# Optimization experiments

Measured on AMD Instinct MI355X. Metric: run time of the kernel, lower is better.

## Reference

```python
import jax, jax.numpy as jnp
import numpy as np

B, S, H, V = 16, 128, 512, 50000
N, R = 5, 2          # mem_size, read_heads
Wd = H               # memory cell width
EPS = 1e-6
XI_SIZES = [R * Wd, R, Wd, 1, Wd, Wd, R, 1, 1, 3 * R]
XI = int(np.sum(XI_SIZES))  # 2573


def oneplus(x):
    return 1.0 + jax.nn.softplus(x)


def content_weight(M, k, beta):
    # M: [B,N,Wd], k: [B,R,Wd], beta: [B,R] -> [B,R,N]
    Mn = M / (jnp.linalg.norm(M, axis=-1, keepdims=True) + EPS)
    kn = k / (jnp.linalg.norm(k, axis=-1, keepdims=True) + EPS)
    sim = jnp.einsum('brw,bnw->brn', kn, Mn)
    return jax.nn.softmax(beta[:, :, None] * sim, axis=-1)


def setup_inputs() -> dict:
    key = jax.random.key(0)
    ks = jax.random.split(key, 8)
    emb = jax.random.normal(ks[0], (V, H), jnp.float32) * 0.02
    emb = emb.at[0].set(0.0)  # PAD row
    return {
        'source': jax.random.randint(ks[1], (B, S), 0, V),
        'source_lengths': jax.random.randint(ks[2], (B,), 1, S + 1),
        'emb': emb,
        'W_ih': jax.random.normal(ks[3], (4 * H, H + R * Wd), jnp.float32) * 0.02,
        'W_hh': jax.random.normal(ks[4], (4 * H, H), jnp.float32) * 0.02,
        'b_lstm': jnp.zeros((4 * H,), jnp.float32),
        'W_int': jax.random.normal(ks[5], (H, XI), jnp.float32) * 0.02,
        'b_int': jnp.zeros((XI,), jnp.float32),
        'W_out': jax.random.normal(ks[6], (H + R * Wd, H), jnp.float32) * 0.02,
        'b_out': jnp.zeros((H,), jnp.float32),
    }


def dnc_forward(source, emb, W_ih, W_hh, b_lstm, W_int, b_int, W_out, b_out):
    x_emb = emb[source]  # [B,S,H] embedding lookup
    splits = np.cumsum(XI_SIZES)[:-1]
    eye = jnp.eye(N, dtype=jnp.float32)

    def step(carry, x_t):
        h, c, M, u, p, L, wr, ww, r = carry
        # LSTM controller: input = [embedded token; read vectors]
        xin = jnp.concatenate([x_t, r.reshape(-1, R * Wd)], axis=-1)
        gates = xin @ W_ih.T + h @ W_hh.T + b_lstm
        i_, f_, g_, o_ = jnp.split(gates, 4, axis=-1)
        c = jax.nn.sigmoid(f_) * c + jax.nn.sigmoid(i_) * jnp.tanh(g_)
        h = jax.nn.sigmoid(o_) * jnp.tanh(c)
        # interface vector
        xi = h @ W_int + b_int
        (rk, rb, wk, wb, e, v, fg, ga, gw, pi) = jnp.split(xi, splits, axis=-1)
        rk = rk.reshape(-1, R, Wd)
        rb = oneplus(rb)                       # [B,R]
        wb = oneplus(wb)                       # [B,1]
        e = jax.nn.sigmoid(e)                  # [B,Wd]
        fg = jax.nn.sigmoid(fg)                # [B,R]
        ga = jax.nn.sigmoid(ga)                # [B,1]
        gw = jax.nn.sigmoid(gw)                # [B,1]
        pi = jax.nn.softmax(pi.reshape(-1, R, 3), axis=-1)
        # usage / retention
        psi = jnp.prod(1.0 - fg[:, :, None] * wr, axis=1)        # [B,N]
        u = (u + ww - u * ww) * psi
        # allocation weighting (sort-based, irregular access)
        phi = jnp.argsort(u, axis=-1)
        u_s = jnp.take_along_axis(u, phi, axis=-1)
        excl = jnp.concatenate([jnp.ones_like(u_s[:, :1]), jnp.cumprod(u_s, axis=-1)[:, :-1]], axis=-1)
        a_s = (1.0 - u_s) * excl
        a = jnp.take_along_axis(a_s, jnp.argsort(phi, axis=-1), axis=-1)
        # write weighting
        cw = content_weight(M, wk[:, None, :], wb)[:, 0]         # [B,N]
        ww = gw * (ga * a + (1.0 - ga) * cw)
        # memory write
        M = M * (1.0 - ww[:, :, None] * e[:, None, :]) + ww[:, :, None] * v[:, None, :]
        # temporal link matrix + precedence
        L = (1.0 - ww[:, :, None] - ww[:, None, :]) * L + ww[:, :, None] * p[:, None, :]
        L = L * (1.0 - eye)
        p = (1.0 - ww.sum(-1, keepdims=True)) * p + ww
        # read weightings
        fw = jnp.einsum('bij,brj->bri', L, wr)
        bw = jnp.einsum('bji,brj->bri', L, wr)
        cr = content_weight(M, rk, rb)                           # [B,R,N]
        wr = pi[..., 0:1] * bw + pi[..., 1:2] * cr + pi[..., 2:3] * fw
        r = jnp.einsum('brn,bnw->brw', wr, M)                    # [B,R,Wd]
        out_t = jnp.concatenate([h, r.reshape(-1, R * Wd)], axis=-1) @ W_out + b_out
        return (h, c, M, u, p, L, wr, ww, r), out_t

    z = jnp.zeros
    init = (z((B, H)), z((B, H)), z((B, N, Wd)), z((B, N)), z((B, N)),
            z((B, N, N)), z((B, R, N)), z((B, N)), z((B, R, Wd)))
    (h, c, *_), outs = jax.lax.scan(step, init, jnp.swapaxes(x_emb, 0, 1))
    return jnp.swapaxes(outs, 0, 1), h, c


def reference(source, source_lengths, emb, W_ih, W_hh, b_lstm, W_int, b_int, W_out, b_out):
    outputs, h, c = dnc_forward(source, emb, W_ih, W_hh, b_lstm, W_int, b_int, W_out, b_out)
    return outputs, (h, c)
```

## Files before the change

### kernel.cpp

```cpp
#include <hip/hip_runtime.h>
#include <math.h>

#define EPSC 1e-6f
#define NBLK 128
#define GBLK 64

#define OFF_H     0u
#define OFF_R     16384u
#define OFF_FLAGS 32768u
#define OFF_GO    36864u
#define OFF_XF    40960u
#define OFF_RF    45056u
#define STATE_END 46080u
#define OFF_XI    46080u
#define OFF_GX    95232u
#define OFF_HR    4289536u

typedef float f32x4 __attribute__((ext_vector_type(4)));

__device__ __forceinline__ float sigmf(float x) { return 1.0f / (1.0f + expf(-x)); }
__device__ __forceinline__ float oneplusf(float x) {
    return 1.0f + fmaxf(x, 0.0f) + log1pf(expf(-fabsf(x)));
}

__device__ __forceinline__ void gst(float* p, float v) {
    __hip_atomic_store((unsigned*)p, __float_as_uint(v),
                       __ATOMIC_RELAXED, __HIP_MEMORY_SCOPE_AGENT);
}

__device__ __forceinline__ void ld12(
    f32x4& h0, f32x4& h1, f32x4& h2, f32x4& h3,
    f32x4& r0, f32x4& r1, f32x4& r2, f32x4& r3,
    f32x4& r4, f32x4& r5, f32x4& r6, f32x4& r7,
    const float* ph, const float* pr)
{
    asm volatile(
        "global_load_dwordx4 %0, %12, off sc0 sc1\n\t"
        "global_load_dwordx4 %1, %12, off offset:512 sc0 sc1\n\t"
        "global_load_dwordx4 %2, %12, off offset:1024 sc0 sc1\n\t"
        "global_load_dwordx4 %3, %12, off offset:1536 sc0 sc1\n\t"
        "global_load_dwordx4 %4, %13, off sc0 sc1\n\t"
        "global_load_dwordx4 %5, %13, off offset:512 sc0 sc1\n\t"
        "global_load_dwordx4 %6, %13, off offset:1024 sc0 sc1\n\t"
        "global_load_dwordx4 %7, %13, off offset:1536 sc0 sc1\n\t"
        "global_load_dwordx4 %8, %13, off offset:2048 sc0 sc1\n\t"
        "global_load_dwordx4 %9, %13, off offset:2560 sc0 sc1\n\t"
        "global_load_dwordx4 %10, %13, off offset:3072 sc0 sc1\n\t"
        "global_load_dwordx4 %11, %13, off offset:3584 sc0 sc1\n\t"
        "s_waitcnt vmcnt(0)"
        : "=&v"(h0), "=&v"(h1), "=&v"(h2), "=&v"(h3),
          "=&v"(r0), "=&v"(r1), "=&v"(r2), "=&v"(r3),
          "=&v"(r4), "=&v"(r5), "=&v"(r6), "=&v"(r7)
        : "v"(ph), "v"(pr)
        : "memory");
}

__device__ __forceinline__ void ld4o(
    f32x4& d0, f32x4& d1, f32x4& d2, f32x4& d3, const float* p)
{
    asm volatile(
        "global_load_dwordx4 %0, %4, off sc0 sc1\n\t"
        "global_load_dwordx4 %1, %4, off offset:512 sc0 sc1\n\t"
        "global_load_dwordx4 %2, %4, off offset:1024 sc0 sc1\n\t"
        "global_load_dwordx4 %3, %4, off offset:1536 sc0 sc1\n\t"
        "s_waitcnt vmcnt(0)"
        : "=&v"(d0), "=&v"(d1), "=&v"(d2), "=&v"(d3)
        : "v"(p)
        : "memory");
}

__device__ __forceinline__ void cld3(
    f32x4& d0, f32x4& d1, f32x4& d2,
    const float* p0, const float* p1, const float* p2)
{
    asm volatile(
        "global_load_dwordx4 %0, %3, off sc0 sc1\n\t"
        "global_load_dwordx4 %1, %4, off sc0 sc1\n\t"
        "global_load_dwordx4 %2, %5, off sc0 sc1\n\t"
        "s_waitcnt vmcnt(0)"
        : "=&v"(d0), "=&v"(d1), "=&v"(d2)
        : "v"(p0), "v"(p1), "v"(p2)
        : "memory");
}

__device__ __forceinline__ void gsync(unsigned* flags, unsigned* go, unsigned gen,
                                      int bi, int bl, int g, int tid)
{
    __builtin_amdgcn_s_waitcnt(0);
    __syncthreads();
    if (tid == 0)
        __hip_atomic_store(&flags[bi * 32], gen, __ATOMIC_RELAXED, __HIP_MEMORY_SCOPE_AGENT);
    if (bl == 0) {
        if (tid < GBLK) {
            unsigned v;
            do {
                v = __hip_atomic_load(&flags[(g * GBLK + tid) * 32], __ATOMIC_RELAXED,
                                      __HIP_MEMORY_SCOPE_AGENT);
                if (v < gen) __builtin_amdgcn_s_sleep(1);
            } while (v < gen);
        }
        __syncthreads();
        if (tid < GBLK)
            __hip_atomic_store(&go[(g * GBLK + tid) * 32], gen, __ATOMIC_RELAXED,
                               __HIP_MEMORY_SCOPE_AGENT);
    }
    if (tid == 0) {
        unsigned v;
        do {
            v = __hip_atomic_load(&go[bi * 32], __ATOMIC_RELAXED, __HIP_MEMORY_SCOPE_AGENT);
            if (v < gen) __builtin_amdgcn_s_sleep(1);
        } while (v < gen);
    }
    __syncthreads();
}

template <int K>
__device__ __forceinline__ void blk_reduce(float* v, float (*s_red)[20],
                                           float* outp, int tid)
{
#pragma unroll
    for (int i = 0; i < K; i++) {
        float x = v[i];
        for (int o = 32; o > 0; o >>= 1) x += __shfl_down(x, o, 64);
        if ((tid & 63) == 0) s_red[tid >> 6][i] = x;
    }
    __syncthreads();
    if (tid < K) outp[tid] = s_red[0][tid] + s_red[1][tid] + s_red[2][tid] + s_red[3][tid];
    __syncthreads();
}

__global__ __launch_bounds__(256, 1) void k_main(
    const float* __restrict__ W_ih, const float* __restrict__ W_hh,
    const float* __restrict__ W_int, const float* __restrict__ b_int,
    const float* __restrict__ gx, float* __restrict__ hbuf,
    float* __restrict__ rbuf, float* __restrict__ xib,
    float* __restrict__ hr, float* __restrict__ out,
    unsigned* __restrict__ flags, unsigned* __restrict__ go,
    unsigned* __restrict__ xf, unsigned* __restrict__ rf)
{
    const int tid = threadIdx.x;
    const int bi  = blockIdx.x;
    const int g   = bi >> 6;
    const int bl  = bi & 63;
    const int bg0 = g * 8;

    __shared__ __align__(16) float big_u[13312];
    __shared__ float s_part[1024];
    __shared__ float s_tot[256];
    __shared__ float c_s[64];
    __shared__ __align__(16) float s_M[5][520];
    __shared__ float st_u[5], st_p[5], st_L[25], st_wr[10], st_ww[5];
    __shared__ float s_red[4][20];
    __shared__ float s_rb[2], s_wb, s_fg[2], s_ga, s_gw, s_pi[2][3];
    __shared__ float s_wrold[2][5], s_uu[5], s_a[5], s_wwn[5];
    __shared__ float s_pold[5], s_Lnew[25];
    __shared__ float s_zw[5], s_z[2][5], s_fw[2][5], s_bw[2][5];
    __shared__ float s_dotA[11], s_dotB[17], s_wrnew[2][5];

    if (tid < 64) c_s[tid] = 0.f;
    if (bl < 8) {
        for (int i = tid; i < 5 * 520; i += 256) (&s_M[0][0])[i] = 0.f;
        if (tid < 5)  { st_u[tid] = 0.f; st_p[tid] = 0.f; st_ww[tid] = 0.f; }
        if (tid < 25) st_L[tid] = 0.f;
        if (tid < 10) st_wr[tid] = 0.f;
    }
    __syncthreads();

#pragma unroll 1
    for (int t = 0; t < 128; t++) {
        const float* h_in  = hbuf + (t & 1) * 8192;
        float*       h_out = hbuf + ((t + 1) & 1) * 8192;

        if (tid < 8) {
            unsigned v;
            do {
                v = __hip_atomic_load(&rf[(bg0 + tid) * 32], __ATOMIC_RELAXED,
                                      __HIP_MEMORY_SCOPE_AGENT);
                if (v < (unsigned)t) __builtin_amdgcn_s_sleep(8);
            } while (v < (unsigned)t);
        }
        __syncthreads();

        float gxv;
        {
            int c = tid & 31, b = tid >> 5;
            int col = (c >> 3) * 512 + bl * 8 + (c & 7);
            gxv = gx[((size_t)t * 16 + bg0 + b) * 2048 + col];
        }

        {
            const int b8 = tid >> 5, sg = tid & 31;
            const float* ph = h_in + (bg0 + b8) * 512 + sg * 4;
            const float* pr = rbuf + (bg0 + b8) * 1024 + sg * 4;
            f32x4 h0, h1, h2, h3, r0, r1, r2, r3, r4, r5, r6, r7;
            ld12(h0, h1, h2, h3, r0, r1, r2, r3, r4, r5, r6, r7, ph, pr);
#define STG(kk, D) { int k = (kk); int cc = k / 48; \
                     *(f32x4*)&big_u[b8 * 1664 + cc * 52 + (k - cc * 48)] = D; }
            STG(sg * 4 + 0 * 128, h0)  STG(sg * 4 + 1 * 128, h1)
            STG(sg * 4 + 2 * 128, h2)  STG(sg * 4 + 3 * 128, h3)
            STG(512 + sg * 4 + 0 * 128, r0)  STG(512 + sg * 4 + 1 * 128, r1)
            STG(512 + sg * 4 + 2 * 128, r2)  STG(512 + sg * 4 + 3 * 128, r3)
            STG(512 + sg * 4 + 4 * 128, r4)  STG(512 + sg * 4 + 5 * 128, r5)
            STG(512 + sg * 4 + 6 * 128, r6)  STG(512 + sg * 4 + 7 * 128, r7)
#undef STG
        }
        __syncthreads();

        const int cq = tid & 7;
        const int ks = tid >> 3;
        const int jcol = bl * 8 + cq;
        float acc[4][8];
#pragma unroll
        for (int g_ = 0; g_ < 4; g_++)
#pragma unroll
            for (int b = 0; b < 8; b++) acc[g_][b] = 0.f;
#pragma unroll
        for (int i = 0; i < 12; i++) {
            int kg = ks * 48 + i * 4;
            f32x4 w[4];
#pragma unroll
            for (int g_ = 0; g_ < 4; g_++) {
                const float* wp = (kg < 512)
                    ? W_hh + (size_t)(g_ * 512 + jcol) * 512 + kg
                    : W_ih + (size_t)(g_ * 512 + jcol) * 1536 + kg;
                w[g_] = *(const f32x4*)wp;
            }
#pragma unroll
            for (int b = 0; b < 8; b++) {
                f32x4 xv = *(const f32x4*)&big_u[b * 1664 + ks * 52 + i * 4];
#pragma unroll
                for (int g_ = 0; g_ < 4; g_++) {
                    acc[g_][b] = fmaf(w[g_][0], xv[0], acc[g_][b]);
                    acc[g_][b] = fmaf(w[g_][1], xv[1], acc[g_][b]);
                    acc[g_][b] = fmaf(w[g_][2], xv[2], acc[g_][b]);
                    acc[g_][b] = fmaf(w[g_][3], xv[3], acc[g_][b]);
                }
            }
        }
#pragma unroll
        for (int g_ = 0; g_ < 4; g_++)
#pragma unroll
            for (int b = 0; b < 8; b++) {
                float x = acc[g_][b];
                x += __shfl_xor(x, 8, 64);
                x += __shfl_xor(x, 16, 64);
                x += __shfl_xor(x, 32, 64);
                acc[g_][b] = x;
            }
        {
            int wv = tid >> 6;
            if ((tid & 63) < 8) {
#pragma unroll
                for (int g_ = 0; g_ < 4; g_++)
#pragma unroll
                    for (int b = 0; b < 8; b++)
                        s_part[((wv * 4 + g_) * 8 + cq) * 8 + b] = acc[g_][b];
            }
        }
        __syncthreads();
        {
            int c = tid & 31, b = tid >> 5;
            int g_ = c >> 3, jq = c & 7;
            float tot = gxv;
#pragma unroll
            for (int w = 0; w < 4; w++)
                tot += s_part[((w * 4 + g_) * 8 + jq) * 8 + b];
            s_tot[c * 8 + b] = tot;
        }
        __syncthreads();
        if (tid < 64) {
            int jl = tid & 7, b = tid >> 3;
            float gi  = s_tot[(0 * 8 + jl) * 8 + b];
            float gf  = s_tot[(1 * 8 + jl) * 8 + b];
            float gg  = s_tot[(2 * 8 + jl) * 8 + b];
            float go_ = s_tot[(3 * 8 + jl) * 8 + b];
            float cc = sigmf(gf) * c_s[jl * 8 + b] + sigmf(gi) * tanhf(gg);
            float hh = sigmf(go_) * tanhf(cc);
            c_s[jl * 8 + b] = cc;
            int j = bl * 8 + jl;
            int bgl = bg0 + b;
            gst(h_out + bgl * 512 + j, hh);
            hr[((size_t)t * 16 + bgl) * 1536 + j] = hh;
            if (t == 127) {
                out[1048576 + bgl * 512 + j] = hh;
                out[1048576 + 8192 + bgl * 512 + j] = cc;
            }
        }
        gsync(flags, go, (unsigned)(t + 1), bi, bl, g, tid);

        {
            {
                const int b8 = tid >> 5, s = tid & 31;
                const float* ph = h_out + (bg0 + b8) * 512 + s * 4;
                f32x4 e0, e1, e2, e3;
                ld4o(e0, e1, e2, e3, ph);
#define STX(j, E) { int k = s * 4 + (j) * 128; \
                    *(f32x4*)&big_u[b8 * 592 + (k >> 5) * 36 + (k & 31)] = E; }
                STX(0, e0) STX(1, e1) STX(2, e2) STX(3, e3)
#undef STX
            }
            __syncthreads();
            const int ql  = tid & 15;
            const int kcl = tid >> 4;
#pragma unroll 1
            for (int p = 0; p < 3; p++) {
                if (p == 2 && bl >= 33) break;
                int q0 = p * 1024 + bl * 16;
                int q  = q0 + ql;
                int qc = (q < 2573) ? q : 2572;
                float wxr[32];
#pragma unroll
                for (int i = 0; i < 32; i++)
                    wxr[i] = W_int[(size_t)(kcl * 32 + i) * 2573 + qc];
                float ax[8];
#pragma unroll
                for (int b = 0; b < 8; b++) ax[b] = 0.f;
#pragma unroll
                for (int b = 0; b < 8; b++) {
                    const f32x4* hp = (const f32x4*)&big_u[b * 592 + kcl * 36];
#pragma unroll
                    for (int i4 = 0; i4 < 8; i4++) {
                        f32x4 hv = hp[i4];
                        ax[b] = fmaf(wxr[i4 * 4 + 0], hv[0], ax[b]);
                        ax[b] = fmaf(wxr[i4 * 4 + 1], hv[1], ax[b]);
                        ax[b] = fmaf(wxr[i4 * 4 + 2], hv[2], ax[b]);
                        ax[b] = fmaf(wxr[i4 * 4 + 3], hv[3], ax[b]);
                    }
                }
#pragma unroll
                for (int b = 0; b < 8; b++) {
                    float x = ax[b];
                    x += __shfl_xor(x, 16, 64);
                    x += __shfl_xor(x, 32, 64);
                    ax[b] = x;
                }
                {
                    int wv = tid >> 6;
                    if ((tid & 63) < 16) {
#pragma unroll
                        for (int b = 0; b < 8; b++)
                            s_part[(wv * 16 + ql) * 8 + b] = ax[b];
                    }
                }
                __syncthreads();
                if (tid < 128) {
                    int q_l = tid >> 3, b = tid & 7;
                    int qq = q0 + q_l;
                    if (qq < 2573) {
                        float v = b_int[qq];
#pragma unroll
                        for (int w = 0; w < 4; w++)
                            v += s_part[(w * 16 + q_l) * 8 + b];
                        gst(&xib[(bg0 + b) * 3072 + qq], v);
                    }
                }
                __syncthreads();
            }
        }
        __builtin_amdgcn_s_waitcnt(0);
        __syncthreads();
        if (tid == 0)
            __hip_atomic_store(&xf[bi * 32], (unsigned)(t + 1),
                               __ATOMIC_RELAXED, __HIP_MEMORY_SCOPE_AGENT);

        if (bl < 8) {
            const int bg = bg0 + bl;
            if (tid < GBLK) {
                unsigned v;
                do {
                    v = __hip_atomic_load(&xf[(g * GBLK + tid) * 32], __ATOMIC_RELAXED,
                                          __HIP_MEMORY_SCOPE_AGENT);
                    if (v < (unsigned)(t + 1)) __builtin_amdgcn_s_sleep(2);
                } while (v < (unsigned)(t + 1));
            }
            __syncthreads();
            {
                const float* xs = xib + bg * 3072;
                f32x4 d0, d1, d2;
                cld3(d0, d1, d2,
                     xs + (tid + 0) * 4, xs + (tid + 256) * 4, xs + (tid + 512) * 4);
                *(f32x4*)&big_u[(tid + 0) * 4]   = d0;
                *(f32x4*)&big_u[(tid + 256) * 4] = d1;
                *(f32x4*)&big_u[(tid + 512) * 4] = d2;
            }
            __syncthreads();
            const float* xb = big_u;

            if (tid == 0) {
                s_wb = oneplusf(xb[1538]);
                s_ga = sigmf(xb[2565]);
                s_gw = sigmf(xb[2566]);
            }
            if (tid == 1 || tid == 2) {
                int rr = tid - 1;
                s_rb[rr] = oneplusf(xb[1024 + rr]);
                s_fg[rr] = sigmf(xb[2563 + rr]);
                float z0 = xb[2567 + rr * 3], z1 = xb[2568 + rr * 3], z2 = xb[2569 + rr * 3];
                float mx = fmaxf(z0, fmaxf(z1, z2));
                float e0 = expf(z0 - mx), e1 = expf(z1 - mx), e2 = expf(z2 - mx);
                float s = e0 + e1 + e2;
                s_pi[rr][0] = e0 / s; s_pi[rr][1] = e1 / s; s_pi[rr][2] = e2 / s;
            }
            if (tid >= 32 && tid < 42) { int i = tid - 32; s_wrold[i / 5][i % 5] = st_wr[i]; }
            if (tid >= 64 && tid < 69) { s_pold[tid - 64] = st_p[tid - 64]; }
            __syncthreads();
            if (tid < 5) {
                float psi = (1.f - s_fg[0] * s_wrold[0][tid]) * (1.f - s_fg[1] * s_wrold[1][tid]);
                float un = (st_u[tid] + st_ww[tid] - st_u[tid] * st_ww[tid]) * psi;
                s_uu[tid] = un; st_u[tid] = un;
            }
            __syncthreads();
            if (tid < 5) {
                float excl = 1.f;
#pragma unroll
                for (int m2 = 0; m2 < 5; m2++) {
                    bool before = (s_uu[m2] < s_uu[tid]) || (s_uu[m2] == s_uu[tid] && m2 < tid);
                    if (before) excl *= s_uu[m2];
                }
                s_a[tid] = (1.f - s_uu[tid]) * excl;
            }
            float accA[11];
#pragma unroll
            for (int i = 0; i < 11; i++) accA[i] = 0.f;
            for (int w = tid; w < 512; w += 256) {
                float wk = xb[1026 + w];
                accA[10] += wk * wk;
#pragma unroll
                for (int n = 0; n < 5; n++) {
                    float m_ = s_M[n][w];
                    accA[n]     += m_ * m_;
                    accA[5 + n] += wk * m_;
                }
            }
            blk_reduce<11>(accA, s_red, s_dotA, tid);
            if (tid < 5) {
                float sim = s_dotA[5 + tid] /
                            ((sqrtf(s_dotA[10]) + EPSC) * (sqrtf(s_dotA[tid]) + EPSC));
                s_zw[tid] = s_wb * sim;
            }
            __syncthreads();
            if (tid < 5) {
                float mx = s_zw[0];
#pragma unroll
                for (int m2 = 1; m2 < 5; m2++) mx = fmaxf(mx, s_zw[m2]);
                float sum = 0.f;
#pragma unroll
                for (int m2 = 0; m2 < 5; m2++) sum += expf(s_zw[m2] - mx);
                float cw = expf(s_zw[tid] - mx) / sum;
                float w_ = s_gw * (s_ga * s_a[tid] + (1.f - s_ga) * cw);
                s_wwn[tid] = w_; st_ww[tid] = w_;
            }
            __syncthreads();
            float accB[17];
#pragma unroll
            for (int i = 0; i < 17; i++) accB[i] = 0.f;
            for (int w = tid; w < 512; w += 256) {
                float ew = sigmf(xb[1539 + w]);
                float vw = xb[2051 + w];
                float rk0 = xb[w], rk1 = xb[512 + w];
                accB[15] += rk0 * rk0; accB[16] += rk1 * rk1;
#pragma unroll
                for (int n = 0; n < 5; n++) {
                    float m_ = s_M[n][w];
                    float mn_ = m_ * (1.f - s_wwn[n] * ew) + s_wwn[n] * vw;
                    s_M[n][w] = mn_;
                    accB[n]      += mn_ * mn_;
                    accB[5 + n]  += rk0 * mn_;
                    accB[10 + n] += rk1 * mn_;
                }
            }
            blk_reduce<17>(accB, s_red, s_dotB, tid);
            if (tid < 25) {
                int i2 = tid / 5, j2 = tid % 5;
                float Ln = (i2 == j2) ? 0.f
                         : (1.f - s_wwn[i2] - s_wwn[j2]) * st_L[tid] + s_wwn[i2] * s_pold[j2];
                s_Lnew[tid] = Ln; st_L[tid] = Ln;
            }
            __syncthreads();
            if (tid < 5) {
                float wsum = s_wwn[0] + s_wwn[1] + s_wwn[2] + s_wwn[3] + s_wwn[4];
                st_p[tid] = (1.f - wsum) * s_pold[tid] + s_wwn[tid];
            }
            if (tid < 10) {
                int rr = tid / 5, ii = tid % 5;
                float fw = 0.f, bw = 0.f;
#pragma unroll
                for (int j2 = 0; j2 < 5; j2++) {
                    fw += s_Lnew[ii * 5 + j2] * s_wrold[rr][j2];
                    bw += s_Lnew[j2 * 5 + ii] * s_wrold[rr][j2];
                }
                s_fw[rr][ii] = fw; s_bw[rr][ii] = bw;
                float sim = s_dotB[5 + rr * 5 + ii] /
                            ((sqrtf(s_dotB[15 + rr]) + EPSC) * (sqrtf(s_dotB[ii]) + EPSC));
                s_z[rr][ii] = s_rb[rr] * sim;
            }
            __syncthreads();
            if (tid < 10) {
                int rr = tid / 5, ii = tid % 5;
                float mx = s_z[rr][0];
#pragma unroll
                for (int m2 = 1; m2 < 5; m2++) mx = fmaxf(mx, s_z[rr][m2]);
                float sum = 0.f;
#pragma unroll
                for (int m2 = 0; m2 < 5; m2++) sum += expf(s_z[rr][m2] - mx);
                float cr = expf(s_z[rr][ii] - mx) / sum;
                float wn = s_pi[rr][0] * s_bw[rr][ii] + s_pi[rr][1] * cr + s_pi[rr][2] * s_fw[rr][ii];
                s_wrnew[rr][ii] = wn; st_wr[rr * 5 + ii] = wn;
            }
            __syncthreads();
            for (int idx = tid; idx < 1024; idx += 256) {
                int rr = idx >> 9, w = idx & 511;
                float rv = 0.f;
#pragma unroll
                for (int n = 0; n < 5; n++) rv += s_wrnew[rr][n] * s_M[n][w];
                gst(&rbuf[bg * 1024 + idx], rv);
                hr[((size_t)t * 16 + bg) * 1536 + 512 + idx] = rv;
            }
            __builtin_amdgcn_s_waitcnt(0);
            __syncthreads();
            if (tid == 0)
                __hip_atomic_store(&rf[bg * 32], (unsigned)(t + 1),
                                   __ATOMIC_RELAXED, __HIP_MEMORY_SCOPE_AGENT);
        }
    }
}

__global__ __launch_bounds__(256) void k_embgx(
    const int* __restrict__ src, const float* __restrict__ emb,
    const float* __restrict__ W_ih, const float* __restrict__ b_lstm,
    float* __restrict__ gx)
{
    __shared__ __align__(16) float As[16][68];
    __shared__ __align__(16) float Bs[16][68];
    const int tid = threadIdx.x;
    const int bm = blockIdx.x, bn = blockIdx.y;
    const int tm = tid >> 4, tn = tid & 15;
    float acc[4][4] = {};
    for (int k0 = 0; k0 < 512; k0 += 16) {
#pragma unroll
        for (int i = 0; i < 4; i++) {
            int idx = tid + 256 * i;
            int m = idx >> 4, kk = idx & 15;
            int tok = bm * 64 + m;
            int row = src[(tok & 15) * 128 + (tok >> 4)];
            As[kk][m] = emb[(size_t)row * 512 + k0 + kk];
        }
#pragma unroll
        for (int i = 0; i < 4; i++) {
            int idx = tid + 256 * i;
            int n = idx >> 4, kk = idx & 15;
            Bs[kk][n] = W_ih[(size_t)(bn * 64 + n) * 1536 + k0 + kk];
        }
        __syncthreads();
#pragma unroll
        for (int kk = 0; kk < 16; kk++) {
            float4 av = *(const float4*)&As[kk][tm * 4];
            float4 bv = *(const float4*)&Bs[kk][tn * 4];
            float a[4] = {av.x, av.y, av.z, av.w};
            float b[4] = {bv.x, bv.y, bv.z, bv.w};
#pragma unroll
            for (int i = 0; i < 4; i++)
#pragma unroll
                for (int j = 0; j < 4; j++) acc[i][j] = fmaf(a[i], b[j], acc[i][j]);
        }
        __syncthreads();
    }
#pragma unroll
    for (int i = 0; i < 4; i++) {
        int tok = bm * 64 + tm * 4 + i;
#pragma unroll
        for (int j = 0; j < 4; j++) {
            int col = bn * 64 + tn * 4 + j;
            gx[(size_t)tok * 2048 + col] = acc[i][j] + b_lstm[col];
        }
    }
}

__global__ __launch_bounds__(256) void k_out(
    const float* __restrict__ hr, const float* __restrict__ W_out,
    const float* __restrict__ b_out, float* __restrict__ out)
{
    __shared__ __align__(16) float As[16][68];
    __shared__ __align__(16) float Bs[16][68];
    const int tid = threadIdx.x;
    const int bm = blockIdx.x, bn = blockIdx.y;
    const int tm = tid >> 4, tn = tid & 15;
    float acc[4][4] = {};
    for (int k0 = 0; k0 < 1536; k0 += 16) {
#pragma unroll
        for (int i = 0; i < 4; i++) {
            int idx = tid + 256 * i;
            int m = idx >> 4, kk = idx & 15;
            As[kk][m] = hr[(size_t)(bm * 64 + m) * 1536 + k0 + kk];
        }
#pragma unroll
        for (int i = 0; i < 4; i++) {
            int idx = tid + 256 * i;
            int kk = idx >> 6, n = idx & 63;
            Bs[kk][n] = W_out[(size_t)(k0 + kk) * 512 + bn * 64 + n];
        }
        __syncthreads();
#pragma unroll
        for (int kk = 0; kk < 16; kk++) {
            float4 av = *(const float4*)&As[kk][tm * 4];
            float4 bv = *(const float4*)&Bs[kk][tn * 4];
            float a[4] = {av.x, av.y, av.z, av.w};
            float b[4] = {bv.x, bv.y, bv.z, bv.w};
#pragma unroll
            for (int i = 0; i < 4; i++)
#pragma unroll
                for (int j = 0; j < 4; j++) acc[i][j] = fmaf(a[i], b[j], acc[i][j]);
        }
        __syncthreads();
    }
#pragma unroll
    for (int i = 0; i < 4; i++) {
        int tok = bm * 64 + tm * 4 + i;
        int b_ = tok & 15, s_ = tok >> 4;
#pragma unroll
        for (int j = 0; j < 4; j++) {
            int qn = bn * 64 + tn * 4 + j;
            out[(size_t)((b_ << 7) + s_) * 512 + qn] = acc[i][j] + b_out[qn];
        }
    }
}

extern "C" void kernel_launch(void* const* d_in, const int* in_sizes, int n_in,
                              void* d_out, int out_size, void* d_ws, size_t ws_size,
                              hipStream_t stream)
{
    const int*   src    = (const int*)d_in[0];
    const float* emb    = (const float*)d_in[2];
    const float* W_ih   = (const float*)d_in[3];
    const float* W_hh   = (const float*)d_in[4];
    const float* b_lstm = (const float*)d_in[5];
    const float* W_int  = (const float*)d_in[6];
    const float* b_int  = (const float*)d_in[7];
    const float* W_out  = (const float*)d_in[8];
    const float* b_out  = (const float*)d_in[9];

    float* ws  = (float*)d_ws;
    float* out = (float*)d_out;

    float*    hbuf  = ws + OFF_H;
    float*    rbuf  = ws + OFF_R;
    unsigned* flags = (unsigned*)(ws + OFF_FLAGS);
    unsigned* go    = (unsigned*)(ws + OFF_GO);
    unsigned* xf    = (unsigned*)(ws + OFF_XF);
    unsigned* rf    = (unsigned*)(ws + OFF_RF);
    float*    xib   = ws + OFF_XI;
    float*    gx    = ws + OFF_GX;
    float*    hrb   = ws + OFF_HR;

    hipMemsetAsync(ws, 0, STATE_END * sizeof(float), stream);

    k_embgx<<<dim3(32, 32), 256, 0, stream>>>(src, emb, W_ih, b_lstm, gx);

    k_main<<<dim3(NBLK), dim3(256), 0, stream>>>(
        W_ih, W_hh, W_int, b_int, gx, hbuf, rbuf, xib, hrb, out,
        flags, go, xf, rf);

    k_out<<<dim3(32, 8), 256, 0, stream>>>(hrb, W_out, b_out, out);
}
```

Baseline: 4.089 ms.

## Precompute W_hh·h for next step while waiting for memory-read results

The recurrent gate GEMM is split so that the h-dependent part (W_hh·h) for step t+1 is computed at the end of step t, right after h is produced, instead of after waiting on the read-vector flag. Only the W_ih·r part remains on the critical path after the rbuf wait. The interface vector is moved into its own shared buffer so it no longer aliases big_u, which now holds the prefetched h. The spin-wait sleep is also shortened. The cost is more shared memory, plus accumulators kept live across the loop, which raises register pressure. It also relies on h_out being visible to the prefetching blocks at that point.

```diff
diff --git a/kernel.cpp b/kernel.cpp
--- a/kernel.cpp
+++ b/kernel.cpp
@@ -28,30 +28,23 @@
                        __ATOMIC_RELAXED, __HIP_MEMORY_SCOPE_AGENT);
 }
 
-__device__ __forceinline__ void ld12(
-    f32x4& h0, f32x4& h1, f32x4& h2, f32x4& h3,
+__device__ __forceinline__ void ld8r(
     f32x4& r0, f32x4& r1, f32x4& r2, f32x4& r3,
-    f32x4& r4, f32x4& r5, f32x4& r6, f32x4& r7,
-    const float* ph, const float* pr)
+    f32x4& r4, f32x4& r5, f32x4& r6, f32x4& r7, const float* pr)
 {
     asm volatile(
-        "global_load_dwordx4 %0, %12, off sc0 sc1\n\t"
-        "global_load_dwordx4 %1, %12, off offset:512 sc0 sc1\n\t"
-        "global_load_dwordx4 %2, %12, off offset:1024 sc0 sc1\n\t"
-        "global_load_dwordx4 %3, %12, off offset:1536 sc0 sc1\n\t"
-        "global_load_dwordx4 %4, %13, off sc0 sc1\n\t"
-        "global_load_dwordx4 %5, %13, off offset:512 sc0 sc1\n\t"
-        "global_load_dwordx4 %6, %13, off offset:1024 sc0 sc1\n\t"
-        "global_load_dwordx4 %7, %13, off offset:1536 sc0 sc1\n\t"
-        "global_load_dwordx4 %8, %13, off offset:2048 sc0 sc1\n\t"
-        "global_load_dwordx4 %9, %13, off offset:2560 sc0 sc1\n\t"
-        "global_load_dwordx4 %10, %13, off offset:3072 sc0 sc1\n\t"
-        "global_load_dwordx4 %11, %13, off offset:3584 sc0 sc1\n\t"
+        "global_load_dwordx4 %0, %8, off sc0 sc1\n\t"
+        "global_load_dwordx4 %1, %8, off offset:512 sc0 sc1\n\t"
+        "global_load_dwordx4 %2, %8, off offset:1024 sc0 sc1\n\t"
+        "global_load_dwordx4 %3, %8, off offset:1536 sc0 sc1\n\t"
+        "global_load_dwordx4 %4, %8, off offset:2048 sc0 sc1\n\t"
+        "global_load_dwordx4 %5, %8, off offset:2560 sc0 sc1\n\t"
+        "global_load_dwordx4 %6, %8, off offset:3072 sc0 sc1\n\t"
+        "global_load_dwordx4 %7, %8, off offset:3584 sc0 sc1\n\t"
         "s_waitcnt vmcnt(0)"
-        : "=&v"(h0), "=&v"(h1), "=&v"(h2), "=&v"(h3),
-          "=&v"(r0), "=&v"(r1), "=&v"(r2), "=&v"(r3),
+        : "=&v"(r0), "=&v"(r1), "=&v"(r2), "=&v"(r3),
           "=&v"(r4), "=&v"(r5), "=&v"(r6), "=&v"(r7)
-        : "v"(ph), "v"(pr)
+        : "v"(pr)
         : "memory");
 }
 
@@ -145,6 +138,7 @@
     const int bg0 = g * 8;
 
     __shared__ __align__(16) float big_u[13312];
+    __shared__ __align__(16) float s_xi[3072];
     __shared__ float s_part[1024];
     __shared__ float s_tot[256];
     __shared__ float c_s[64];
@@ -166,9 +160,20 @@
     }
     __syncthreads();
 
+    const int cq = tid & 7;
+    const int ks = tid >> 3;
+    const int jcol = bl * 8 + cq;
+    const int npre = (ks < 10) ? 12 : ((ks == 10) ? 8 : 0);
+    const int b8 = tid >> 5, sg = tid & 31;
+
+    float acc[4][8];
+#pragma unroll
+    for (int g_ = 0; g_ < 4; g_++)
+#pragma unroll
+        for (int b = 0; b < 8; b++) acc[g_][b] = 0.f;
+
 #pragma unroll 1
     for (int t = 0; t < 128; t++) {
-        const float* h_in  = hbuf + (t & 1) * 8192;
         float*       h_out = hbuf + ((t + 1) & 1) * 8192;
 
         if (tid < 8) {
@@ -176,7 +181,7 @@
             do {
                 v = __hip_atomic_load(&rf[(bg0 + tid) * 32], __ATOMIC_RELAXED,
                                       __HIP_MEMORY_SCOPE_AGENT);
-                if (v < (unsigned)t) __builtin_amdgcn_s_sleep(8);
+                if (v < (unsigned)t) __builtin_amdgcn_s_sleep(4);
             } while (v < (unsigned)t);
         }
         __syncthreads();
@@ -187,44 +192,24 @@
             int col = (c >> 3) * 512 + bl * 8 + (c & 7);
             gxv = gx[((size_t)t * 16 + bg0 + b) * 2048 + col];
         }
-
         {
-            const int b8 = tid >> 5, sg = tid & 31;
-            const float* ph = h_in + (bg0 + b8) * 512 + sg * 4;
             const float* pr = rbuf + (bg0 + b8) * 1024 + sg * 4;
-            f32x4 h0, h1, h2, h3, r0, r1, r2, r3, r4, r5, r6, r7;
-            ld12(h0, h1, h2, h3, r0, r1, r2, r3, r4, r5, r6, r7, ph, pr);
+            f32x4 r0, r1, r2, r3, r4, r5, r6, r7;
+            ld8r(r0, r1, r2, r3, r4, r5, r6, r7, pr);
 #define STG(kk, D) { int k = (kk); int cc = k / 48; \
                      *(f32x4*)&big_u[b8 * 1664 + cc * 52 + (k - cc * 48)] = D; }
-            STG(sg * 4 + 0 * 128, h0)  STG(sg * 4 + 1 * 128, h1)
-            STG(sg * 4 + 2 * 128, h2)  STG(sg * 4 + 3 * 128, h3)
             STG(512 + sg * 4 + 0 * 128, r0)  STG(512 + sg * 4 + 1 * 128, r1)
             STG(512 + sg * 4 + 2 * 128, r2)  STG(512 + sg * 4 + 3 * 128, r3)
             STG(512 + sg * 4 + 4 * 128, r4)  STG(512 + sg * 4 + 5 * 128, r5)
             STG(512 + sg * 4 + 6 * 128, r6)  STG(512 + sg * 4 + 7 * 128, r7)
-#undef STG
-        }
-        __syncthreads();
-
-        const int cq = tid & 7;
-        const int ks = tid >> 3;
-        const int jcol = bl * 8 + cq;
-        float acc[4][8];
-#pragma unroll
-        for (int g_ = 0; g_ < 4; g_++)
-#pragma unroll
-            for (int b = 0; b < 8; b++) acc[g_][b] = 0.f;
-#pragma unroll
-        for (int i = 0; i < 12; i++) {
+        }
+        __syncthreads();
+        for (int i = npre; i < 12; i++) {
             int kg = ks * 48 + i * 4;
             f32x4 w[4];
 #pragma unroll
-            for (int g_ = 0; g_ < 4; g_++) {
-                const float* wp = (kg < 512)
-                    ? W_hh + (size_t)(g_ * 512 + jcol) * 512 + kg
-                    : W_ih + (size_t)(g_ * 512 + jcol) * 1536 + kg;
-                w[g_] = *(const f32x4*)wp;
-            }
+            for (int g_ = 0; g_ < 4; g_++)
+                w[g_] = *(const f32x4*)(W_ih + (size_t)(g_ * 512 + jcol) * 1536 + kg);
 #pragma unroll
             for (int b = 0; b < 8; b++) {
                 f32x4 xv = *(const f32x4*)&big_u[b * 1664 + ks * 52 + i * 4];
@@ -290,11 +275,10 @@
 
         {
             {
-                const int b8 = tid >> 5, s = tid & 31;
-                const float* ph = h_out + (bg0 + b8) * 512 + s * 4;
+                const float* ph = h_out + (bg0 + b8) * 512 + sg * 4;
                 f32x4 e0, e1, e2, e3;
                 ld4o(e0, e1, e2, e3, ph);
-#define STX(j, E) { int k = s * 4 + (j) * 128; \
+#define STX(j, E) { int k = sg * 4 + (j) * 128; \
                     *(f32x4*)&big_u[b8 * 592 + (k >> 5) * 36 + (k & 31)] = E; }
                 STX(0, e0) STX(1, e1) STX(2, e2) STX(3, e3)
 #undef STX
@@ -379,12 +363,12 @@
                 f32x4 d0, d1, d2;
                 cld3(d0, d1, d2,
                      xs + (tid + 0) * 4, xs + (tid + 256) * 4, xs + (tid + 512) * 4);
-                *(f32x4*)&big_u[(tid + 0) * 4]   = d0;
-                *(f32x4*)&big_u[(tid + 256) * 4] = d1;
-                *(f32x4*)&big_u[(tid + 512) * 4] = d2;
-            }
-            __syncthreads();
-            const float* xb = big_u;
+                *(f32x4*)&s_xi[(tid + 0) * 4]   = d0;
+                *(f32x4*)&s_xi[(tid + 256) * 4] = d1;
+                *(f32x4*)&s_xi[(tid + 512) * 4] = d2;
+            }
+            __syncthreads();
+            const float* xb = s_xi;
 
             if (tid == 0) {
                 s_wb = oneplusf(xb[1538]);
@@ -522,6 +506,40 @@
                 __hip_atomic_store(&rf[bg * 32], (unsigned)(t + 1),
                                    __ATOMIC_RELAXED, __HIP_MEMORY_SCOPE_AGENT);
         }
+
+#pragma unroll
+        for (int g_ = 0; g_ < 4; g_++)
+#pragma unroll
+            for (int b = 0; b < 8; b++) acc[g_][b] = 0.f;
+        if (t < 127) {
+            {
+                const float* ph = h_out + (bg0 + b8) * 512 + sg * 4;
+                f32x4 e0, e1, e2, e3;
+                ld4o(e0, e1, e2, e3, ph);
+                STG(sg * 4 + 0 * 128, e0)  STG(sg * 4 + 1 * 128, e1)
+                STG(sg * 4 + 2 * 128, e2)  STG(sg * 4 + 3 * 128, e3)
+#undef STG
+            }
+            __syncthreads();
+            for (int i = 0; i < npre; i++) {
+                int kg = ks * 48 + i * 4;
+                f32x4 w[4];
+#pragma unroll
+                for (int g_ = 0; g_ < 4; g_++)
+                    w[g_] = *(const f32x4*)(W_hh + (size_t)(g_ * 512 + jcol) * 512 + kg);
+#pragma unroll
+                for (int b = 0; b < 8; b++) {
+                    f32x4 xv = *(const f32x4*)&big_u[b * 1664 + ks * 52 + i * 4];
+#pragma unroll
+                    for (int g_ = 0; g_ < 4; g_++) {
+                        acc[g_][b] = fmaf(w[g_][0], xv[0], acc[g_][b]);
+                        acc[g_][b] = fmaf(w[g_][1], xv[1], acc[g_][b]);
+                        acc[g_][b] = fmaf(w[g_][2], xv[2], acc[g_][b]);
+                        acc[g_][b] = fmaf(w[g_][3], xv[3], acc[g_][b]);
+                    }
+                }
+            }
+        }
     }
 }
 
```

After: 4.881 ms. +19.4%, slower.

## Split batch across four groups of 64 blocks instead of two

Applied to the files above, without the earlier changes.

Doubles the persistent grid from 128 to 256 blocks, so each 64-block group handles 4 batch rows instead of 8. Per-block LSTM gate and interface matmul work is halved, and all buffer offsets, loads, accumulators and reductions are resized to match. The xi staging moves to its own shared array so it no longer aliases big_u. The trade-off is that every block still streams the same W_hh/W_ih/W_int slices, so total weight traffic doubles, and twice as many blocks take part in the flag-based cross-block sync.

```diff
diff --git a/kernel.cpp b/kernel.cpp
--- a/kernel.cpp
+++ b/kernel.cpp
@@ -2,19 +2,19 @@
 #include <math.h>
 
 #define EPSC 1e-6f
-#define NBLK 128
+#define NBLK 256
 #define GBLK 64
 
 #define OFF_H     0u
 #define OFF_R     16384u
 #define OFF_FLAGS 32768u
-#define OFF_GO    36864u
-#define OFF_XF    40960u
-#define OFF_RF    45056u
-#define STATE_END 46080u
-#define OFF_XI    46080u
-#define OFF_GX    95232u
-#define OFF_HR    4289536u
+#define OFF_GO    40960u
+#define OFF_XF    49152u
+#define OFF_RF    57344u
+#define STATE_END 58368u
+#define OFF_XI    58368u
+#define OFF_GX    107520u
+#define OFF_HR    4301824u
 
 typedef float f32x4 __attribute__((ext_vector_type(4)));
 
@@ -28,43 +28,31 @@
                        __ATOMIC_RELAXED, __HIP_MEMORY_SCOPE_AGENT);
 }
 
-__device__ __forceinline__ void ld12(
-    f32x4& h0, f32x4& h1, f32x4& h2, f32x4& h3,
+__device__ __forceinline__ void ld6g(
+    f32x4& h0, f32x4& h1,
     f32x4& r0, f32x4& r1, f32x4& r2, f32x4& r3,
-    f32x4& r4, f32x4& r5, f32x4& r6, f32x4& r7,
     const float* ph, const float* pr)
 {
     asm volatile(
-        "global_load_dwordx4 %0, %12, off sc0 sc1\n\t"
-        "global_load_dwordx4 %1, %12, off offset:512 sc0 sc1\n\t"
-        "global_load_dwordx4 %2, %12, off offset:1024 sc0 sc1\n\t"
-        "global_load_dwordx4 %3, %12, off offset:1536 sc0 sc1\n\t"
-        "global_load_dwordx4 %4, %13, off sc0 sc1\n\t"
-        "global_load_dwordx4 %5, %13, off offset:512 sc0 sc1\n\t"
-        "global_load_dwordx4 %6, %13, off offset:1024 sc0 sc1\n\t"
-        "global_load_dwordx4 %7, %13, off offset:1536 sc0 sc1\n\t"
-        "global_load_dwordx4 %8, %13, off offset:2048 sc0 sc1\n\t"
-        "global_load_dwordx4 %9, %13, off offset:2560 sc0 sc1\n\t"
-        "global_load_dwordx4 %10, %13, off offset:3072 sc0 sc1\n\t"
-        "global_load_dwordx4 %11, %13, off offset:3584 sc0 sc1\n\t"
+        "global_load_dwordx4 %0, %6, off sc0 sc1\n\t"
+        "global_load_dwordx4 %1, %6, off offset:1024 sc0 sc1\n\t"
+        "global_load_dwordx4 %2, %7, off sc0 sc1\n\t"
+        "global_load_dwordx4 %3, %7, off offset:1024 sc0 sc1\n\t"
+        "global_load_dwordx4 %4, %7, off offset:2048 sc0 sc1\n\t"
+        "global_load_dwordx4 %5, %7, off offset:3072 sc0 sc1\n\t"
         "s_waitcnt vmcnt(0)"
-        : "=&v"(h0), "=&v"(h1), "=&v"(h2), "=&v"(h3),
-          "=&v"(r0), "=&v"(r1), "=&v"(r2), "=&v"(r3),
-          "=&v"(r4), "=&v"(r5), "=&v"(r6), "=&v"(r7)
+        : "=&v"(h0), "=&v"(h1), "=&v"(r0), "=&v"(r1), "=&v"(r2), "=&v"(r3)
         : "v"(ph), "v"(pr)
         : "memory");
 }
 
-__device__ __forceinline__ void ld4o(
-    f32x4& d0, f32x4& d1, f32x4& d2, f32x4& d3, const float* p)
+__device__ __forceinline__ void ld2h(f32x4& d0, f32x4& d1, const float* p)
 {
     asm volatile(
-        "global_load_dwordx4 %0, %4, off sc0 sc1\n\t"
-        "global_load_dwordx4 %1, %4, off offset:512 sc0 sc1\n\t"
-        "global_load_dwordx4 %2, %4, off offset:1024 sc0 sc1\n\t"
-        "global_load_dwordx4 %3, %4, off offset:1536 sc0 sc1\n\t"
+        "global_load_dwordx4 %0, %2, off sc0 sc1\n\t"
+        "global_load_dwordx4 %1, %2, off offset:1024 sc0 sc1\n\t"
         "s_waitcnt vmcnt(0)"
-        : "=&v"(d0), "=&v"(d1), "=&v"(d2), "=&v"(d3)
+        : "=&v"(d0), "=&v"(d1)
         : "v"(p)
         : "memory");
 }
@@ -142,12 +130,13 @@
     const int bi  = blockIdx.x;
     const int g   = bi >> 6;
     const int bl  = bi & 63;
-    const int bg0 = g * 8;
-
-    __shared__ __align__(16) float big_u[13312];
-    __shared__ float s_part[1024];
-    __shared__ float s_tot[256];
-    __shared__ float c_s[64];
+    const int bg0 = g * 4;
+
+    __shared__ __align__(16) float big_u[6656];
+    __shared__ __align__(16) float s_xi[3072];
+    __shared__ float s_part[512];
+    __shared__ float s_tot[128];
+    __shared__ float c_s[32];
     __shared__ __align__(16) float s_M[5][520];
     __shared__ float st_u[5], st_p[5], st_L[25], st_wr[10], st_ww[5];
     __shared__ float s_red[4][20];
@@ -157,8 +146,8 @@
     __shared__ float s_zw[5], s_z[2][5], s_fw[2][5], s_bw[2][5];
     __shared__ float s_dotA[11], s_dotB[17], s_wrnew[2][5];
 
-    if (tid < 64) c_s[tid] = 0.f;
-    if (bl < 8) {
+    if (tid < 32) c_s[tid] = 0.f;
+    if (bl < 4) {
         for (int i = tid; i < 5 * 520; i += 256) (&s_M[0][0])[i] = 0.f;
         if (tid < 5)  { st_u[tid] = 0.f; st_p[tid] = 0.f; st_ww[tid] = 0.f; }
         if (tid < 25) st_L[tid] = 0.f;
@@ -166,54 +155,51 @@
     }
     __syncthreads();
 
+    const int cq = tid & 7;
+    const int ks = tid >> 3;
+    const int jcol = bl * 8 + cq;
+    const int b4 = tid >> 6, sg = tid & 63;
+
 #pragma unroll 1
     for (int t = 0; t < 128; t++) {
         const float* h_in  = hbuf + (t & 1) * 8192;
         float*       h_out = hbuf + ((t + 1) & 1) * 8192;
 
-        if (tid < 8) {
+        float gxv = 0.f;
+        if (tid < 128) {
+            int c = tid & 31, b = tid >> 5;
+            int col = (c >> 3) * 512 + bl * 8 + (c & 7);
+            gxv = gx[((size_t)t * 16 + bg0 + b) * 2048 + col];
+        }
+        if (tid < 4) {
             unsigned v;
             do {
                 v = __hip_atomic_load(&rf[(bg0 + tid) * 32], __ATOMIC_RELAXED,
                                       __HIP_MEMORY_SCOPE_AGENT);
-                if (v < (unsigned)t) __builtin_amdgcn_s_sleep(8);
+                if (v < (unsigned)t) __builtin_amdgcn_s_sleep(4);
             } while (v < (unsigned)t);
         }
         __syncthreads();
 
-        float gxv;
         {
-            int c = tid & 31, b = tid >> 5;
-            int col = (c >> 3) * 512 + bl * 8 + (c & 7);
-            gxv = gx[((size_t)t * 16 + bg0 + b) * 2048 + col];
-        }
-
-        {
-            const int b8 = tid >> 5, sg = tid & 31;
-            const float* ph = h_in + (bg0 + b8) * 512 + sg * 4;
-            const float* pr = rbuf + (bg0 + b8) * 1024 + sg * 4;
-            f32x4 h0, h1, h2, h3, r0, r1, r2, r3, r4, r5, r6, r7;
-            ld12(h0, h1, h2, h3, r0, r1, r2, r3, r4, r5, r6, r7, ph, pr);
+            const float* ph = h_in + (bg0 + b4) * 512 + sg * 4;
+            const float* pr = rbuf + (bg0 + b4) * 1024 + sg * 4;
+            f32x4 h0, h1, r0, r1, r2, r3;
+            ld6g(h0, h1, r0, r1, r2, r3, ph, pr);
 #define STG(kk, D) { int k = (kk); int cc = k / 48; \
-                     *(f32x4*)&big_u[b8 * 1664 + cc * 52 + (k - cc * 48)] = D; }
-            STG(sg * 4 + 0 * 128, h0)  STG(sg * 4 + 1 * 128, h1)
-            STG(sg * 4 + 2 * 128, h2)  STG(sg * 4 + 3 * 128, h3)
-            STG(512 + sg * 4 + 0 * 128, r0)  STG(512 + sg * 4 + 1 * 128, r1)
-            STG(512 + sg * 4 + 2 * 128, r2)  STG(512 + sg * 4 + 3 * 128, r3)
-            STG(512 + sg * 4 + 4 * 128, r4)  STG(512 + sg * 4 + 5 * 128, r5)
-            STG(512 + sg * 4 + 6 * 128, r6)  STG(512 + sg * 4 + 7 * 128, r7)
+                     *(f32x4*)&big_u[b4 * 1664 + cc * 52 + (k - cc * 48)] = D; }
+            STG(sg * 4 + 0 * 256, h0)        STG(sg * 4 + 1 * 256, h1)
+            STG(512 + sg * 4 + 0 * 256, r0)  STG(512 + sg * 4 + 1 * 256, r1)
+            STG(512 + sg * 4 + 2 * 256, r2)  STG(512 + sg * 4 + 3 * 256, r3)
 #undef STG
         }
         __syncthreads();
 
-        const int cq = tid & 7;
-        const int ks = tid >> 3;
-        const int jcol = bl * 8 + cq;
-        float acc[4][8];
+        float acc[4][4];
 #pragma unroll
         for (int g_ = 0; g_ < 4; g_++)
 #pragma unroll
-            for (int b = 0; b < 8; b++) acc[g_][b] = 0.f;
+            for (int b = 0; b < 4; b++) acc[g_][b] = 0.f;
 #pragma unroll
         for (int i = 0; i < 12; i++) {
             int kg = ks * 48 + i * 4;
@@ -226,7 +212,7 @@
                 w[g_] = *(const f32x4*)wp;
             }
 #pragma unroll
-            for (int b = 0; b < 8; b++) {
+            for (int b = 0; b < 4; b++) {
                 f32x4 xv = *(const f32x4*)&big_u[b * 1664 + ks * 52 + i * 4];
 #pragma unroll
                 for (int g_ = 0; g_ < 4; g_++) {
@@ -240,7 +226,7 @@
 #pragma unroll
         for (int g_ = 0; g_ < 4; g_++)
 #pragma unroll
-            for (int b = 0; b < 8; b++) {
+            for (int b = 0; b < 4; b++) {
                 float x = acc[g_][b];
                 x += __shfl_xor(x, 8, 64);
                 x += __shfl_xor(x, 16, 64);
@@ -253,30 +239,30 @@
 #pragma unroll
                 for (int g_ = 0; g_ < 4; g_++)
 #pragma unroll
-                    for (int b = 0; b < 8; b++)
-                        s_part[((wv * 4 + g_) * 8 + cq) * 8 + b] = acc[g_][b];
-            }
-        }
-        __syncthreads();
-        {
+                    for (int b = 0; b < 4; b++)
+                        s_part[((wv * 4 + g_) * 8 + cq) * 4 + b] = acc[g_][b];
+            }
+        }
+        __syncthreads();
+        if (tid < 128) {
             int c = tid & 31, b = tid >> 5;
             int g_ = c >> 3, jq = c & 7;
             float tot = gxv;
 #pragma unroll
             for (int w = 0; w < 4; w++)
-                tot += s_part[((w * 4 + g_) * 8 + jq) * 8 + b];
-            s_tot[c * 8 + b] = tot;
-        }
-        __syncthreads();
-        if (tid < 64) {
+                tot += s_part[((w * 4 + g_) * 8 + jq) * 4 + b];
+            s_tot[c * 4 + b] = tot;
+        }
+        __syncthreads();
+        if (tid < 32) {
             int jl = tid & 7, b = tid >> 3;
-            float gi  = s_tot[(0 * 8 + jl) * 8 + b];
-            float gf  = s_tot[(1 * 8 + jl) * 8 + b];
-            float gg  = s_tot[(2 * 8 + jl) * 8 + b];
-            float go_ = s_tot[(3 * 8 + jl) * 8 + b];
-            float cc = sigmf(gf) * c_s[jl * 8 + b] + sigmf(gi) * tanhf(gg);
+            float gi  = s_tot[(0 * 8 + jl) * 4 + b];
+            float gf  = s_tot[(1 * 8 + jl) * 4 + b];
+            float gg  = s_tot[(2 * 8 + jl) * 4 + b];
+            float go_ = s_tot[(3 * 8 + jl) * 4 + b];
+            float cc = sigmf(gf) * c_s[jl * 4 + b] + sigmf(gi) * tanhf(gg);
             float hh = sigmf(go_) * tanhf(cc);
-            c_s[jl * 8 + b] = cc;
+            c_s[jl * 4 + b] = cc;
             int j = bl * 8 + jl;
             int bgl = bg0 + b;
             gst(h_out + bgl * 512 + j, hh);
@@ -290,13 +276,12 @@
 
         {
             {
-                const int b8 = tid >> 5, s = tid & 31;
-                const float* ph = h_out + (bg0 + b8) * 512 + s * 4;
-                f32x4 e0, e1, e2, e3;
-                ld4o(e0, e1, e2, e3, ph);
-#define STX(j, E) { int k = s * 4 + (j) * 128; \
-                    *(f32x4*)&big_u[b8 * 592 + (k >> 5) * 36 + (k & 31)] = E; }
-                STX(0, e0) STX(1, e1) STX(2, e2) STX(3, e3)
+                const float* ph = h_out + (bg0 + b4) * 512 + sg * 4;
+                f32x4 e0, e1;
+                ld2h(e0, e1, ph);
+#define STX(j, E) { int k = sg * 4 + (j) * 256; \
+                    *(f32x4*)&big_u[b4 * 592 + (k >> 5) * 36 + (k & 31)] = E; }
+                STX(0, e0) STX(1, e1)
 #undef STX
             }
             __syncthreads();
@@ -312,11 +297,11 @@
 #pragma unroll
                 for (int i = 0; i < 32; i++)
                     wxr[i] = W_int[(size_t)(kcl * 32 + i) * 2573 + qc];
-                float ax[8];
-#pragma unroll
-                for (int b = 0; b < 8; b++) ax[b] = 0.f;
-#pragma unroll
-                for (int b = 0; b < 8; b++) {
+                float ax[4];
+#pragma unroll
+                for (int b = 0; b < 4; b++) ax[b] = 0.f;
+#pragma unroll
+                for (int b = 0; b < 4; b++) {
                     const f32x4* hp = (const f32x4*)&big_u[b * 592 + kcl * 36];
 #pragma unroll
                     for (int i4 = 0; i4 < 8; i4++) {
@@ -328,7 +313,7 @@
                     }
                 }
 #pragma unroll
-                for (int b = 0; b < 8; b++) {
+                for (int b = 0; b < 4; b++) {
                     float x = ax[b];
                     x += __shfl_xor(x, 16, 64);
                     x += __shfl_xor(x, 32, 64);
@@ -338,19 +323,19 @@
                     int wv = tid >> 6;
                     if ((tid & 63) < 16) {
 #pragma unroll
-                        for (int b = 0; b < 8; b++)
-                            s_part[(wv * 16 + ql) * 8 + b] = ax[b];
+                        for (int b = 0; b < 4; b++)
+                            s_part[(wv * 16 + ql) * 4 + b] = ax[b];
                     }
                 }
                 __syncthreads();
-                if (tid < 128) {
-                    int q_l = tid >> 3, b = tid & 7;
+                if (tid < 64) {
+                    int q_l = tid >> 2, b = tid & 3;
                     int qq = q0 + q_l;
                     if (qq < 2573) {
                         float v = b_int[qq];
 #pragma unroll
                         for (int w = 0; w < 4; w++)
-                            v += s_part[(w * 16 + q_l) * 8 + b];
+                            v += s_part[(w * 16 + q_l) * 4 + b];
                         gst(&xib[(bg0 + b) * 3072 + qq], v);
                     }
                 }
@@ -363,7 +348,7 @@
             __hip_atomic_store(&xf[bi * 32], (unsigned)(t + 1),
                                __ATOMIC_RELAXED, __HIP_MEMORY_SCOPE_AGENT);
 
-        if (bl < 8) {
+        if (bl < 4) {
             const int bg = bg0 + bl;
             if (tid < GBLK) {
                 unsigned v;
@@ -379,12 +364,12 @@
                 f32x4 d0, d1, d2;
                 cld3(d0, d1, d2,
                      xs + (tid + 0) * 4, xs + (tid + 256) * 4, xs + (tid + 512) * 4);
-                *(f32x4*)&big_u[(tid + 0) * 4]   = d0;
-                *(f32x4*)&big_u[(tid + 256) * 4] = d1;
-                *(f32x4*)&big_u[(tid + 512) * 4] = d2;
-            }
-            __syncthreads();
-            const float* xb = big_u;
+                *(f32x4*)&s_xi[(tid + 0) * 4]   = d0;
+                *(f32x4*)&s_xi[(tid + 256) * 4] = d1;
+                *(f32x4*)&s_xi[(tid + 512) * 4] = d2;
+            }
+            __syncthreads();
+            const float* xb = s_xi;
 
             if (tid == 0) {
                 s_wb = oneplusf(xb[1538]);
```

Result: faster. 3.665 ms (-10.4%).
